# Performance work log

Measured on AMD Instinct MI355X. Metric: run time of the kernel, lower is better.

## Reference

```python
import jax, jax.numpy as jnp
import numpy as np

N = 4096
HID = 256
H = 4
D = HID // H  # 64
EDGE_DIM = 16
DEG = 32
E = N * DEG
EPS = 1e-5


def _layer_norm(x, g, b):
    m = jnp.mean(x, axis=-1, keepdims=True)
    v = jnp.mean((x - m) ** 2, axis=-1, keepdims=True)
    return (x - m) * jax.lax.rsqrt(v + EPS) * g + b


def setup_inputs() -> dict:
    key = jax.random.key(0)
    ks = jax.random.split(key, 16)
    s = 1.0 / np.sqrt(HID)
    x = jax.random.normal(ks[0], (N, HID), dtype=jnp.float32)
    # ring graph: every node is a src with DEG distinct neighbors -> no empty
    # softmax rows, no duplicate (src, dst) pairs
    src = jnp.repeat(jnp.arange(N, dtype=jnp.int64), DEG)
    dst = (src + jnp.tile(jnp.arange(1, DEG + 1, dtype=jnp.int64), N)) % N
    edge_index = jnp.stack([src, dst], axis=0)
    edge_attr = jax.random.normal(ks[1], (E, EDGE_DIM), dtype=jnp.float32)
    inp = {
        "x": x,
        "edge_index": edge_index,
        "edge_attr": edge_attr,
        "Wq": jax.random.uniform(ks[2], (HID, HID), jnp.float32, -s, s),
        "bq": jnp.zeros((HID,), jnp.float32),
        "Wk": jax.random.uniform(ks[3], (HID, HID), jnp.float32, -s, s),
        "bk": jnp.zeros((HID,), jnp.float32),
        "Wv": jax.random.uniform(ks[4], (HID, HID), jnp.float32, -s, s),
        "bv": jnp.zeros((HID,), jnp.float32),
        "Wo": jax.random.uniform(ks[5], (HID, HID), jnp.float32, -s, s),
        "bo": jnp.zeros((HID,), jnp.float32),
        "We": jax.random.uniform(ks[6], (EDGE_DIM, H), jnp.float32, -1.0 / np.sqrt(EDGE_DIM), 1.0 / np.sqrt(EDGE_DIM)),
        "be": jnp.zeros((H,), jnp.float32),
        "g1": jnp.ones((HID,), jnp.float32),
        "b1": jnp.zeros((HID,), jnp.float32),
        "g2": jnp.ones((HID,), jnp.float32),
        "b2": jnp.zeros((HID,), jnp.float32),
        "Wf1": jax.random.uniform(ks[7], (HID, 4 * HID), jnp.float32, -s, s),
        "bf1": jnp.zeros((4 * HID,), jnp.float32),
        "Wf2": jax.random.uniform(ks[8], (4 * HID, HID), jnp.float32, -1.0 / np.sqrt(4 * HID), 1.0 / np.sqrt(4 * HID)),
        "bf2": jnp.zeros((HID,), jnp.float32),
    }
    return inp


def reference(x, edge_index, edge_attr, Wq, bq, Wk, bk, Wv, bv, Wo, bo,
              We, be, g1, b1, g2, b2, Wf1, bf1, Wf2, bf2):
    src, dst = edge_index[0], edge_index[1]
    q = (x @ Wq + bq).reshape(N, H, D)
    k = (x @ Wk + bk).reshape(N, H, D)
    v = (x @ Wv + bv).reshape(N, H, D)
    edge_bias = edge_attr @ We + be                       # [E, H]
    dot = jnp.sum(q[src] * k[dst], axis=-1) / np.sqrt(D)  # [E, H]
    total_bias = dot + edge_bias                          # [E, H]
    # dense (H, N, N) logits, -inf everywhere except the E edges (as in the
    # original module)
    logits = jnp.full((H, N, N), -jnp.inf, dtype=x.dtype)
    logits = logits.at[:, src, dst].set(total_bias.T)
    attn = jax.nn.softmax(logits, axis=-1)                # [H, N, N]
    out = jnp.einsum('hnm,mhd->nhd', attn, v).reshape(N, HID)
    out = out @ Wo + bo
    x = _layer_norm(x + out, g1, b1)
    ffn = jax.nn.relu(x @ Wf1 + bf1) @ Wf2 + bf2
    x = _layer_norm(x + ffn, g2, b2)
    return x
```

## Files before the change

### kernel.cpp

```cpp
#include <hip/hip_runtime.h>
#include <cstddef>

#define N_NODES 4096
#define HIDDEN  256
#define NHEAD   4
#define DHEAD   64
#define EDGE_DIM 16
#define DEG     32
#define NEDGE   (N_NODES * DEG)
#define LN_EPS  1e-5f
#define QKV_STRIDE 768
#define KV_WIN  47

typedef short  s16x8 __attribute__((ext_vector_type(8)));
typedef float  f32x4 __attribute__((ext_vector_type(4)));
typedef unsigned short u16x8 __attribute__((ext_vector_type(8)));
typedef unsigned short u16x4 __attribute__((ext_vector_type(4)));

__device__ __forceinline__ unsigned short f2b(float f) {
    union { float f; unsigned u; } c{f};
    unsigned u = c.u;
    return (unsigned short)((u + 0x7fffu + ((u >> 16) & 1u)) >> 16);
}
__device__ __forceinline__ float b2f(unsigned short s) {
    union { unsigned u; float f; } c;
    c.u = ((unsigned)s) << 16;
    return c.f;
}
__device__ __forceinline__ int xcd_swz(int bid, int total) {
    const int q = total >> 3;
    return (bid & 7) * q + (bid >> 3);
}

__device__ __forceinline__ void pack_tile(const float* __restrict__ src,
                                          unsigned short* __restrict__ dst,
                                          int K, int Nn, int tt, int rowoff,
                                          float (*tile)[65], int tid) {
    const int tk = K / 64;
    const int k0 = (tt % tk) * 64, n0 = (tt / tk) * 64;

    const int kk = tid >> 2, nq = (tid & 3) * 16;
#pragma unroll
    for (int i = 0; i < 16; i += 4) {
        float4 vv = *(const float4*)&src[(size_t)(k0 + kk) * Nn + n0 + nq + i];
        tile[kk][nq + i + 0] = vv.x;
        tile[kk][nq + i + 1] = vv.y;
        tile[kk][nq + i + 2] = vv.z;
        tile[kk][nq + i + 3] = vv.w;
    }
    __syncthreads();
    const int nn = tid >> 2, kq = (tid & 3) * 16;
    unsigned short tmp[16];
#pragma unroll
    for (int i = 0; i < 16; ++i) tmp[i] = f2b(tile[kq + i][nn]);
    unsigned short* drow = dst + (size_t)(rowoff + n0 + nn) * K + k0 + kq;
    *(u16x8*)(drow + 0) = *(u16x8*)&tmp[0];
    *(u16x8*)(drow + 8) = *(u16x8*)&tmp[8];
}

__global__ __launch_bounds__(256) void pack_kernel(
    const float* __restrict__ Wq, const float* __restrict__ Wk,
    const float* __restrict__ Wv, const float* __restrict__ Wo,
    const float* __restrict__ Wf1, const float* __restrict__ Wf2,
    const float* __restrict__ bq, const float* __restrict__ bk,
    const float* __restrict__ bv,
    unsigned short* __restrict__ Wqkv_t, unsigned short* __restrict__ Wo_t,
    unsigned short* __restrict__ Wf1_t, unsigned short* __restrict__ Wf2_t,
    float* __restrict__ bias768) {
    const int b = blockIdx.x;
    const int tid = threadIdx.x;
    __shared__ float tile[64][65];

    if (b < 48) {
        int m = b / 16, tt = b % 16;
        const float* src = (m == 0) ? Wq : ((m == 1) ? Wk : Wv);
        pack_tile(src, Wqkv_t, 256, 256, tt, m * 256, tile, tid);
    } else if (b < 64) {
        pack_tile(Wo, Wo_t, 256, 256, b - 48, 0, tile, tid);
    } else if (b < 128) {
        pack_tile(Wf1, Wf1_t, 256, 1024, b - 64, 0, tile, tid);
    } else if (b < 192) {
        pack_tile(Wf2, Wf2_t, 1024, 256, b - 128, 0, tile, tid);
    } else {
        bias768[tid]       = bq[tid];
        bias768[256 + tid] = bk[tid];
        bias768[512 + tid] = bv[tid];
    }
}

__global__ __launch_bounds__(256) void gemm_qkv(const float* __restrict__ X,
                                                const unsigned short* __restrict__ Bt,
                                                const float* __restrict__ bias,
                                                unsigned short* __restrict__ Cout) {
    __shared__ unsigned short sA[64 * 64];
    __shared__ unsigned short sB[96 * 64];
    const int tid = threadIdx.x;
    const int wave = tid >> 6, lane = tid & 63;
    const int b2 = xcd_swz(blockIdx.x, 512);
    const int row0 = (b2 >> 3) * 64, col0 = (b2 & 7) * 96;
    const int wr = wave >> 1, wc = wave & 1;

    f32x4 acc[2][3] = {};

    const int ar  = tid >> 2;
    const int akb = (tid & 3) * 16;
    const int acb = akb * 2;
    const int axr = (ar & 7) << 4;
    const int aso0 = (ar * 128) | ((acb +  0) ^ axr);
    const int aso1 = (ar * 128) | ((acb + 16) ^ axr);

    float4 f0, f1, f2v, f3;
    s16x8 breg[3];

#define QKV_LOAD(KT)                                                          \
    {                                                                         \
        const float* Ap = X + (size_t)(row0 + ar) * 256 + (KT) * 64 + akb;    \
        f0  = *(const float4*)(Ap + 0);                                       \
        f1  = *(const float4*)(Ap + 4);                                       \
        f2v = *(const float4*)(Ap + 8);                                       \
        f3  = *(const float4*)(Ap + 12);                                      \
        const char* Bb = (const char*)Bt + ((size_t)col0 * 256 + (KT) * 64) * 2; \
        _Pragma("unroll")                                                     \
        for (int p = 0; p < 3; ++p) {                                         \
            const int lo = tid * 16 + p * 4096;                               \
            const int r = lo >> 7, c = lo & 127;                              \
            breg[p] = *(const s16x8*)(Bb + (size_t)r * 512 + c);              \
        }                                                                     \
    }

    QKV_LOAD(0);
#pragma unroll
    for (int kt = 0; kt < 4; ++kt) {
        if (kt) __syncthreads();
        u16x8 pa0 = {f2b(f0.x), f2b(f0.y), f2b(f0.z), f2b(f0.w),
                     f2b(f1.x), f2b(f1.y), f2b(f1.z), f2b(f1.w)};
        u16x8 pa1 = {f2b(f2v.x), f2b(f2v.y), f2b(f2v.z), f2b(f2v.w),
                     f2b(f3.x), f2b(f3.y), f2b(f3.z), f2b(f3.w)};
        *(u16x8*)((char*)sA + aso0) = pa0;
        *(u16x8*)((char*)sA + aso1) = pa1;
#pragma unroll
        for (int p = 0; p < 3; ++p) {
            const int lo = tid * 16 + p * 4096;
            const int r = lo >> 7, c = lo & 127;
            const int so = (lo & ~127) | (c ^ ((r & 7) << 4));
            *(s16x8*)((char*)sB + so) = breg[p];
        }
        __syncthreads();
        if (kt < 3) QKV_LOAD(kt + 1);

        const char* sAc = (const char*)sA;
        const char* sBc = (const char*)sB;
#pragma unroll
        for (int kk = 0; kk < 64; kk += 32) {
            const int koffb = (kk + ((lane >> 4) << 3)) * 2;
            s16x8 a[2], bfr[3];
#pragma unroll
            for (int m = 0; m < 2; ++m) {
                const int r = wr * 32 + m * 16 + (lane & 15);
                int off = r * 128 + koffb;
                off ^= (r & 7) << 4;
                a[m] = *(const s16x8*)(sAc + off);
            }
#pragma unroll
            for (int n = 0; n < 3; ++n) {
                const int c = wc * 48 + n * 16 + (lane & 15);
                int off = c * 128 + koffb;
                off ^= (c & 7) << 4;
                bfr[n] = *(const s16x8*)(sBc + off);
            }
#pragma unroll
            for (int m = 0; m < 2; ++m)
#pragma unroll
                for (int n = 0; n < 3; ++n)
                    acc[m][n] = __builtin_amdgcn_mfma_f32_16x16x32_bf16(
                        a[m], bfr[n], acc[m][n], 0, 0, 0);
        }
    }
#undef QKV_LOAD

    const int crow = row0 + wr * 32 + ((lane >> 4) << 2);
    const int ccol = col0 + wc * 48 + (lane & 15);
#pragma unroll
    for (int n = 0; n < 3; ++n) {
        const int c = ccol + n * 16;
        const float bv = bias[c];
#pragma unroll
        for (int m = 0; m < 2; ++m)
#pragma unroll
            for (int j = 0; j < 4; ++j)
                Cout[(size_t)(crow + m * 16 + j) * QKV_STRIDE + c] =
                    f2b(acc[m][n][j] + bv);
    }
}

__global__ __launch_bounds__(256) void gemm_ffn1(const unsigned short* __restrict__ A,
                                                 const unsigned short* __restrict__ Bt,
                                                 const float* __restrict__ bias,
                                                 unsigned short* __restrict__ Cout) {
    constexpr int K = 256;
    __shared__ unsigned short sA[64 * 64];
    __shared__ unsigned short sB[128 * 64];
    const int tid = threadIdx.x;
    const int wave = tid >> 6, lane = tid & 63;
    const int b2 = xcd_swz(blockIdx.x, 512);
    const int row0 = (b2 >> 3) * 64, col0 = (b2 & 7) * 128;
    const int wr = wave >> 1, wc = wave & 1;

    f32x4 acc[2][4] = {};

    const int lo0 = tid * 16, lo1 = lo0 + 4096;
    const int r0 = lo0 >> 7, c0 = lo0 & 127;
    const int r1 = lo1 >> 7, c1 = lo1 & 127;
    const int so0 = (lo0 & ~127) | (c0 ^ ((r0 & 7) << 4));
    const int so1 = (lo1 & ~127) | (c1 ^ ((r1 & 7) << 4));

    s16x8 a0r, a1r, breg[4];

#define F1_LOAD(KT)                                                           \
    {                                                                         \
        const char* Ab = (const char*)A + ((size_t)row0 * K + (KT) * 64) * 2; \
        a0r = *(const s16x8*)(Ab + (size_t)r0 * (K * 2) + c0);                \
        a1r = *(const s16x8*)(Ab + (size_t)r1 * (K * 2) + c1);                \
        const char* Bb = (const char*)Bt + ((size_t)col0 * K + (KT) * 64) * 2;\
        _Pragma("unroll")                                                     \
        for (int p = 0; p < 4; ++p) {                                         \
            const int lo = tid * 16 + p * 4096;                               \
            const int r = lo >> 7, c = lo & 127;                              \
            breg[p] = *(const s16x8*)(Bb + (size_t)r * (K * 2) + c);          \
        }                                                                     \
    }

    F1_LOAD(0);
#pragma unroll
    for (int kt = 0; kt < 4; ++kt) {
        if (kt) __syncthreads();
        *(s16x8*)((char*)sA + so0) = a0r;
        *(s16x8*)((char*)sA + so1) = a1r;
#pragma unroll
        for (int p = 0; p < 4; ++p) {
            const int lo = tid * 16 + p * 4096;
            const int r = lo >> 7, c = lo & 127;
            const int so = (lo & ~127) | (c ^ ((r & 7) << 4));
            *(s16x8*)((char*)sB + so) = breg[p];
        }
        __syncthreads();
        if (kt + 1 < 4) F1_LOAD(kt + 1);

        const char* sAc = (const char*)sA;
        const char* sBc = (const char*)sB;
#pragma unroll
        for (int kk = 0; kk < 64; kk += 32) {
            const int koffb = (kk + ((lane >> 4) << 3)) * 2;
            s16x8 a[2], bfr[4];
#pragma unroll
            for (int m = 0; m < 2; ++m) {
                const int r = wr * 32 + m * 16 + (lane & 15);
                int off = r * 128 + koffb;
                off ^= (r & 7) << 4;
                a[m] = *(const s16x8*)(sAc + off);
            }
#pragma unroll
            for (int n = 0; n < 4; ++n) {
                const int c = wc * 64 + n * 16 + (lane & 15);
                int off = c * 128 + koffb;
                off ^= (c & 7) << 4;
                bfr[n] = *(const s16x8*)(sBc + off);
            }
#pragma unroll
            for (int m = 0; m < 2; ++m)
#pragma unroll
                for (int n = 0; n < 4; ++n)
                    acc[m][n] = __builtin_amdgcn_mfma_f32_16x16x32_bf16(
                        a[m], bfr[n], acc[m][n], 0, 0, 0);
        }
    }
#undef F1_LOAD

    const int crow = row0 + wr * 32 + ((lane >> 4) << 2);
    const int ccol = col0 + wc * 64 + (lane & 15);
#pragma unroll
    for (int n = 0; n < 4; ++n) {
        const int c = ccol + n * 16;
        const float bv = bias[c];
#pragma unroll
        for (int m = 0; m < 2; ++m)
#pragma unroll
            for (int j = 0; j < 4; ++j) {
                const int r = crow + m * 16 + j;
                Cout[(size_t)r * 1024 + c] = f2b(fmaxf(acc[m][n][j] + bv, 0.f));
            }
    }
}

__global__ __launch_bounds__(256) void gemm_partial(const unsigned short* __restrict__ A,
                                                    const unsigned short* __restrict__ Bt,
                                                    float* __restrict__ part) {
    constexpr int KF = 1024;
    __shared__ unsigned short sA[64 * 64];
    __shared__ unsigned short sB[64 * 64];
    const int tid = threadIdx.x;
    const int wave = tid >> 6, lane = tid & 63;
    const int b2 = xcd_swz(blockIdx.x, 512);
    const int z = b2 >> 8;
    const int rem = b2 & 255;
    const int row0 = (rem >> 2) * 64, col0 = (rem & 3) * 64;
    const int wr = wave >> 1, wc = wave & 1;

    f32x4 acc[2][2] = {};

    const int lo0 = tid * 16;
    const int lo1 = lo0 + 4096;
    const int r0 = lo0 >> 7, c0 = lo0 & 127;
    const int r1 = lo1 >> 7, c1 = lo1 & 127;
    const int so0 = (lo0 & ~127) | (c0 ^ ((r0 & 7) << 4));
    const int so1 = (lo1 & ~127) | (c1 ^ ((r1 & 7) << 4));

    const char* Abase = (const char*)A + ((size_t)row0 * KF + z * 512) * 2;
    const char* Bbase = (const char*)Bt + ((size_t)col0 * KF + z * 512) * 2;

    s16x8 a0r, a1r, b0r, b1r;

#define GP_LOAD(KT)                                                           \
    {                                                                         \
        a0r = *(const s16x8*)(Abase + (KT) * 128 + (size_t)r0 * (KF * 2) + c0); \
        a1r = *(const s16x8*)(Abase + (KT) * 128 + (size_t)r1 * (KF * 2) + c1); \
        b0r = *(const s16x8*)(Bbase + (KT) * 128 + (size_t)r0 * (KF * 2) + c0); \
        b1r = *(const s16x8*)(Bbase + (KT) * 128 + (size_t)r1 * (KF * 2) + c1); \
    }

    GP_LOAD(0);
#pragma unroll
    for (int kt = 0; kt < 8; ++kt) {
        if (kt) __syncthreads();
        *(s16x8*)((char*)sA + so0) = a0r;
        *(s16x8*)((char*)sA + so1) = a1r;
        *(s16x8*)((char*)sB + so0) = b0r;
        *(s16x8*)((char*)sB + so1) = b1r;
        __syncthreads();
        if (kt + 1 < 8) GP_LOAD(kt + 1);

        const char* sAc = (const char*)sA;
        const char* sBc = (const char*)sB;
#pragma unroll
        for (int kk = 0; kk < 64; kk += 32) {
            const int koffb = (kk + ((lane >> 4) << 3)) * 2;
            s16x8 a[2], bfr[2];
#pragma unroll
            for (int m = 0; m < 2; ++m) {
                const int r = wr * 32 + m * 16 + (lane & 15);
                int off = r * 128 + koffb;
                off ^= (r & 7) << 4;
                a[m] = *(const s16x8*)(sAc + off);
            }
#pragma unroll
            for (int n = 0; n < 2; ++n) {
                const int c = wc * 32 + n * 16 + (lane & 15);
                int off = c * 128 + koffb;
                off ^= (c & 7) << 4;
                bfr[n] = *(const s16x8*)(sBc + off);
            }
#pragma unroll
            for (int m = 0; m < 2; ++m)
#pragma unroll
                for (int n = 0; n < 2; ++n)
                    acc[m][n] = __builtin_amdgcn_mfma_f32_16x16x32_bf16(
                        a[m], bfr[n], acc[m][n], 0, 0, 0);
        }
    }
#undef GP_LOAD

    const int crow = row0 + wr * 32 + ((lane >> 4) << 2);
    const int ccol = col0 + wc * 32 + (lane & 15);
    float* pz = part + (size_t)z * N_NODES * HIDDEN;
#pragma unroll
    for (int n = 0; n < 2; ++n) {
        const int c = ccol + n * 16;
#pragma unroll
        for (int m = 0; m < 2; ++m)
#pragma unroll
            for (int j = 0; j < 4; ++j)
                pz[(size_t)(crow + m * 16 + j) * HIDDEN + c] = acc[m][n][j];
    }
}

__global__ __launch_bounds__(256) void ln2_reduce(const float* __restrict__ part,
                                                  const unsigned short* __restrict__ yb,
                                                  const float* __restrict__ bf2,
                                                  const float* __restrict__ g2,
                                                  const float* __restrict__ b2,
                                                  float* __restrict__ out) {
    const int tid = threadIdx.x;
    const int row = blockIdx.x * 8 + (tid >> 5);
    const int cb = (tid & 31) * 8;
    const size_t rb = (size_t)row * HIDDEN;
    constexpr size_t ZS = (size_t)N_NODES * HIDDEN;

    u16x8 yv = *(const u16x8*)&yb[rb + cb];
    float vals[8];
#pragma unroll
    for (int q = 0; q < 2; ++q) {
        const int c = cb + q * 4;
        float4 vb = *(const float4*)&bf2[c];
        float4 s0 = *(const float4*)&part[0 * ZS + rb + c];
        float4 s1 = *(const float4*)&part[1 * ZS + rb + c];
        vals[q * 4 + 0] = b2f(yv[q * 4 + 0]) + vb.x + s0.x + s1.x;
        vals[q * 4 + 1] = b2f(yv[q * 4 + 1]) + vb.y + s0.y + s1.y;
        vals[q * 4 + 2] = b2f(yv[q * 4 + 2]) + vb.z + s0.z + s1.z;
        vals[q * 4 + 3] = b2f(yv[q * 4 + 3]) + vb.w + s0.w + s1.w;
    }
    float sm = 0.f, sq = 0.f;
#pragma unroll
    for (int i = 0; i < 8; ++i) { sm += vals[i]; sq = fmaf(vals[i], vals[i], sq); }
#pragma unroll
    for (int off = 16; off >= 1; off >>= 1) {
        sm += __shfl_xor(sm, off);
        sq += __shfl_xor(sq, off);
    }
    const float mean = sm * (1.f / HIDDEN);
    const float var  = sq * (1.f / HIDDEN) - mean * mean;
    const float inv  = rsqrtf(var + LN_EPS);
#pragma unroll
    for (int q = 0; q < 2; ++q) {
        const int c = cb + q * 4;
        float4 vg = *(const float4*)&g2[c];
        float4 vbb = *(const float4*)&b2[c];
        float4 o;
        o.x = (vals[q * 4 + 0] - mean) * inv * vg.x + vbb.x;
        o.y = (vals[q * 4 + 1] - mean) * inv * vg.y + vbb.y;
        o.z = (vals[q * 4 + 2] - mean) * inv * vg.z + vbb.z;
        o.w = (vals[q * 4 + 3] - mean) * inv * vg.w + vbb.w;
        *(float4*)&out[rb + c] = o;
    }
}

__global__ __launch_bounds__(512) void attn_oproj_ln(
    const unsigned short* __restrict__ qkv,
    const int* __restrict__ edge_dst,
    const float* __restrict__ edge_attr,
    const float* __restrict__ We, const float* __restrict__ be,
    const unsigned short* __restrict__ Wo_t,
    const float* __restrict__ bo,
    const float* __restrict__ x,
    const float* __restrict__ g, const float* __restrict__ b,
    unsigned short* __restrict__ yb) {
    __shared__ float sQ[16][260];
    __shared__ float sP[16][NHEAD][DEG];
    __shared__ int   sDst[16][DEG];
    __shared__ float sWe[EDGE_DIM * NHEAD];
    __shared__ unsigned short sKV[2][KV_WIN * 256];
    __shared__ unsigned short sA[16 * 256];
    __shared__ unsigned short sB[2][256 * 64];
    __shared__ float rs[16][8], rq[16][8];

    const int tid = threadIdx.x;
    const int wave = tid >> 6, lane = tid & 63;
    const int n0 = blockIdx.x * 16;

    {
        const int r = tid >> 5, e = (tid & 31) * 8;
        u16x8 v = *(const u16x8*)(qkv + (size_t)(n0 + r) * QKV_STRIDE + e);
#pragma unroll
        for (int i = 0; i < 8; ++i) sQ[r][e + i] = b2f(v[i]);
    }
    for (int t = tid; t < 2 * KV_WIN * 32; t += 512) {
        const int half = (t >= KV_WIN * 32) ? 1 : 0;
        const int tt = t - half * (KV_WIN * 32);
        const int rr = tt >> 5, c16 = tt & 31;
        const int gsrc = (n0 + 1 + rr) & (N_NODES - 1);
        u16x8 v = *(const u16x8*)(qkv + (size_t)gsrc * QKV_STRIDE +
                                  (half ? 512 : 256) + c16 * 8);
        const int so = rr * 512 + ((c16 ^ (rr & 7)) * 16);
        *(u16x8*)((char*)sKV[half] + so) = v;
    }
    if (tid < EDGE_DIM * NHEAD) sWe[tid] = We[tid];
    __syncthreads();

    {
        const int node = tid >> 5, j = tid & 31;
        const int dstj = edge_dst[(n0 + node) * DEG + j];
        sDst[node][j] = dstj;
        const int idx = (dstj - n0 - 1) & (N_NODES - 1);
        const char* krow = (const char*)sKV[0] + idx * 512;
        const int swz = (idx & 7);
        float lg[4];
#pragma unroll
        for (int h = 0; h < 4; ++h) {
            float dot = 0.f;
            const float* qh = &sQ[node][h * 64];
#pragma unroll
            for (int q8 = 0; q8 < 8; ++q8) {
                const int c16 = h * 8 + q8;
                u16x8 kv = *(const u16x8*)(krow + ((c16 ^ swz) * 16));
#pragma unroll
                for (int d = 0; d < 8; ++d)
                    dot = fmaf(qh[q8 * 8 + d], b2f(kv[d]), dot);
            }
            lg[h] = dot * 0.125f + be[h];
        }
        const float* ea_ = edge_attr + (size_t)((n0 + node) * DEG + j) * EDGE_DIM;
#pragma unroll
        for (int c = 0; c < EDGE_DIM; ++c) {
            const float eav = ea_[c];
#pragma unroll
            for (int h = 0; h < 4; ++h)
                lg[h] = fmaf(eav, sWe[c * NHEAD + h], lg[h]);
        }
#pragma unroll
        for (int h = 0; h < 4; ++h) {
            float mx = lg[h];
#pragma unroll
            for (int off = 16; off >= 1; off >>= 1)
                mx = fmaxf(mx, __shfl_xor(mx, off));
            float p = __expf(lg[h] - mx);
            float sum = p;
#pragma unroll
            for (int off = 16; off >= 1; off >>= 1)
                sum += __shfl_xor(sum, off);
            sP[node][h][j] = p / sum;
        }
    }
    __syncthreads();

    {
        const int node = tid >> 5, oct = tid & 31;
        const int h = oct >> 3;
        const int chunk = oct;
        float acc8[8] = {};
#pragma unroll 8
        for (int j = 0; j < DEG; ++j) {
            const float p = sP[node][h][j];
            const int idx = (sDst[node][j] - n0 - 1) & (N_NODES - 1);
            u16x8 vv = *(const u16x8*)((const char*)sKV[1] + idx * 512 +
                                       ((chunk ^ (idx & 7)) * 16));
#pragma unroll
            for (int i = 0; i < 8; ++i) acc8[i] = fmaf(p, b2f(vv[i]), acc8[i]);
        }
        u16x8 pk;
#pragma unroll
        for (int i = 0; i < 8; ++i) pk[i] = f2b(acc8[i]);
        const int so = node * 512 + ((oct * 16) ^ ((node & 7) << 4));
        *(u16x8*)((char*)sA + so) = pk;
    }

    s16x8 breg[4];
#define WO_LOAD(KT)                                                           \
    {                                                                         \
        _Pragma("unroll")                                                     \
        for (int p = 0; p < 4; ++p) {                                         \
            const int lo = tid * 16 + p * 8192;                               \
            const int r = lo >> 7, c = lo & 127;                              \
            breg[p] = *(const s16x8*)((const char*)Wo_t + (size_t)r * 512 +   \
                                      (KT) * 128 + c);                        \
        }                                                                     \
    }
#define WO_STORE(BUF)                                                         \
    {                                                                         \
        _Pragma("unroll")                                                     \
        for (int p = 0; p < 4; ++p) {                                         \
            const int lo = tid * 16 + p * 8192;                               \
            const int r = lo >> 7, c = lo & 127;                              \
            const int so = (lo & ~127) | (c ^ ((r & 7) << 4));                \
            *(s16x8*)((char*)sB[BUF] + so) = breg[p];                         \
        }                                                                     \
    }

    WO_LOAD(0);
    WO_STORE(0);
    __syncthreads();

    f32x4 acc[2] = {};
#pragma unroll
    for (int kt = 0; kt < 4; ++kt) {
        if (kt + 1 < 4) WO_LOAD(kt + 1);

        const char* sBc = (const char*)sB[kt & 1];
#pragma unroll
        for (int kk = 0; kk < 64; kk += 32) {
            const int lk = ((lane >> 4) << 3);
            s16x8 a;
            {
                const int r = lane & 15;
                const int koffb = (kt * 64 + kk + lk) * 2;
                a = *(const s16x8*)((const char*)sA + r * 512 +
                                    (koffb ^ ((r & 7) << 4)));
            }
            s16x8 bfr[2];
            const int boffb = (kk + lk) * 2;
#pragma unroll
            for (int n = 0; n < 2; ++n) {
                const int c = wave * 32 + n * 16 + (lane & 15);
                bfr[n] = *(const s16x8*)(sBc + c * 128 + (boffb ^ ((c & 7) << 4)));
            }
#pragma unroll
            for (int n = 0; n < 2; ++n)
                acc[n] = __builtin_amdgcn_mfma_f32_16x16x32_bf16(a, bfr[n], acc[n], 0, 0, 0);
        }

        if (kt + 1 < 4) {
            WO_STORE((kt + 1) & 1);
            __syncthreads();
        }
    }
#undef WO_LOAD
#undef WO_STORE

    const int rbase = ((lane >> 4) << 2);
    const int cbase = wave * 32 + (lane & 15);

    float sm[4] = {}, sq_[4] = {};
#pragma unroll
    for (int n = 0; n < 2; ++n) {
        const int c = cbase + n * 16;
        const float bv = bo[c];
#pragma unroll
        for (int j = 0; j < 4; ++j) {
            const int r = rbase + j;
            float v = acc[n][j] + bv + x[(size_t)(n0 + r) * HIDDEN + c];
            acc[n][j] = v;
            sm[j] += v;
            sq_[j] = fmaf(v, v, sq_[j]);
        }
    }
#pragma unroll
    for (int off = 8; off >= 1; off >>= 1) {
#pragma unroll
        for (int j = 0; j < 4; ++j) {
            sm[j] += __shfl_xor(sm[j], off);
            sq_[j] += __shfl_xor(sq_[j], off);
        }
    }
    if ((lane & 15) == 0) {
#pragma unroll
        for (int j = 0; j < 4; ++j) {
            rs[rbase + j][wave] = sm[j];
            rq[rbase + j][wave] = sq_[j];
        }
    }
    __syncthreads();

#pragma unroll
    for (int j = 0; j < 4; ++j) {
        const int r = rbase + j;
        float tot = 0.f, totq = 0.f;
#pragma unroll
        for (int w = 0; w < 8; ++w) { tot += rs[r][w]; totq += rq[r][w]; }
        const float mean = tot * (1.f / HIDDEN);
        const float var  = totq * (1.f / HIDDEN) - mean * mean;
        const float inv  = rsqrtf(var + LN_EPS);
#pragma unroll
        for (int n = 0; n < 2; ++n) {
            const int c = cbase + n * 16;
            const float res = (acc[n][j] - mean) * inv * g[c] + b[c];
            yb[(size_t)(n0 + r) * HIDDEN + c] = f2b(res);
        }
    }
}

extern "C" void kernel_launch(void* const* d_in, const int* in_sizes, int n_in,
                              void* d_out, int out_size, void* d_ws, size_t ws_size,
                              hipStream_t stream) {
    const float* x   = (const float*)d_in[0];
    const int*   ei  = (const int*)d_in[1];
    const float* ea  = (const float*)d_in[2];
    const float* Wq  = (const float*)d_in[3];
    const float* bq  = (const float*)d_in[4];
    const float* Wk  = (const float*)d_in[5];
    const float* bk  = (const float*)d_in[6];
    const float* Wv  = (const float*)d_in[7];
    const float* bv  = (const float*)d_in[8];
    const float* Wo  = (const float*)d_in[9];
    const float* bo  = (const float*)d_in[10];
    const float* We  = (const float*)d_in[11];
    const float* be  = (const float*)d_in[12];
    const float* g1  = (const float*)d_in[13];
    const float* b1  = (const float*)d_in[14];
    const float* g2  = (const float*)d_in[15];
    const float* b2  = (const float*)d_in[16];
    const float* Wf1 = (const float*)d_in[17];
    const float* bf1 = (const float*)d_in[18];
    const float* Wf2 = (const float*)d_in[19];
    const float* bf2 = (const float*)d_in[20];

    char* W = (char*)d_ws;
    unsigned short* Wqkv_t  = (unsigned short*)(W + (2u << 20));
    unsigned short* Wo_t    = (unsigned short*)(W + (2u << 20) + 384 * 1024);
    unsigned short* Wf1_t   = (unsigned short*)(W + (2u << 20) + 512 * 1024);
    unsigned short* Wf2_t   = (unsigned short*)(W + (2u << 20) + 1024 * 1024);
    float*          bias768 = (float*)(W + (2u << 20) + 1536 * 1024);
    unsigned short* qkvb    = (unsigned short*)(W + (4u << 20));
    unsigned short* h1b     = (unsigned short*)(W + (4u << 20));
    unsigned short* yb      = (unsigned short*)(W + (16u << 20));
    float*          part    = (float*)(W + (20u << 20));

    const dim3 blk(256);

    pack_kernel<<<193, blk, 0, stream>>>(Wq, Wk, Wv, Wo, Wf1, Wf2, bq, bk, bv,
                                         Wqkv_t, Wo_t, Wf1_t, Wf2_t, bias768);

    gemm_qkv<<<512, blk, 0, stream>>>(x, Wqkv_t, bias768, qkvb);

    attn_oproj_ln<<<N_NODES / 16, dim3(512), 0, stream>>>(
        qkvb, ei + NEDGE, ea, We, be, Wo_t, bo, x, g1, b1, yb);

    gemm_ffn1<<<512, blk, 0, stream>>>(yb, Wf1_t, bf1, h1b);

    gemm_partial<<<512, blk, 0, stream>>>(h1b, Wf2_t, part);

    ln2_reduce<<<N_NODES / 8, blk, 0, stream>>>(part, yb, bf2, g2, b2, (float*)d_out);
}
```

Measured before the change: 53.54 us.

## Read Wo fragments directly from global and alias sQ/sA to cut LDS

Removes the double-buffered shared-memory staging of Wo in the fused attention+O-proj+LN kernel, so MFMA B fragments are loaded straight from global (L2-resident) Wo_t. The sQ and sA buffers now share one shared-memory region. Launch bounds request 4 blocks per CU. This shrinks LDS use from roughly 130KB to about 64KB so more blocks can be resident, which should hide latency better. The trade-off is uncoalesced, strided global loads for B, and a possible race if sA is written while sQ is still being read without a barrier in between.

New measurement: 54.31 us. About the same (+1.4%).

```diff
diff --git a/kernel.cpp b/kernel.cpp
--- a/kernel.cpp
+++ b/kernel.cpp
@@ -433,7 +433,7 @@
     }
 }
 
-__global__ __launch_bounds__(512) void attn_oproj_ln(
+__global__ __launch_bounds__(512, 4) void attn_oproj_ln(
     const unsigned short* __restrict__ qkv,
     const int* __restrict__ edge_dst,
     const float* __restrict__ edge_attr,
@@ -443,14 +443,15 @@
     const float* __restrict__ x,
     const float* __restrict__ g, const float* __restrict__ b,
     unsigned short* __restrict__ yb) {
-    __shared__ float sQ[16][260];
+    __shared__ __align__(16) char uQA[16 * 260 * 4];
     __shared__ float sP[16][NHEAD][DEG];
     __shared__ int   sDst[16][DEG];
     __shared__ float sWe[EDGE_DIM * NHEAD];
     __shared__ unsigned short sKV[2][KV_WIN * 256];
-    __shared__ unsigned short sA[16 * 256];
-    __shared__ unsigned short sB[2][256 * 64];
     __shared__ float rs[16][8], rq[16][8];
+
+    float (*sQ)[260] = (float(*)[260])uQA;
+    unsigned short* sA = (unsigned short*)uQA;
 
     const int tid = threadIdx.x;
     const int wave = tid >> 6, lane = tid & 63;
@@ -541,68 +542,32 @@
         const int so = node * 512 + ((oct * 16) ^ ((node & 7) << 4));
         *(u16x8*)((char*)sA + so) = pk;
     }
-
-    s16x8 breg[4];
-#define WO_LOAD(KT)                                                           \
-    {                                                                         \
-        _Pragma("unroll")                                                     \
-        for (int p = 0; p < 4; ++p) {                                         \
-            const int lo = tid * 16 + p * 8192;                               \
-            const int r = lo >> 7, c = lo & 127;                              \
-            breg[p] = *(const s16x8*)((const char*)Wo_t + (size_t)r * 512 +   \
-                                      (KT) * 128 + c);                        \
-        }                                                                     \
-    }
-#define WO_STORE(BUF)                                                         \
-    {                                                                         \
-        _Pragma("unroll")                                                     \
-        for (int p = 0; p < 4; ++p) {                                         \
-            const int lo = tid * 16 + p * 8192;                               \
-            const int r = lo >> 7, c = lo & 127;                              \
-            const int so = (lo & ~127) | (c ^ ((r & 7) << 4));                \
-            *(s16x8*)((char*)sB[BUF] + so) = breg[p];                         \
-        }                                                                     \
-    }
-
-    WO_LOAD(0);
-    WO_STORE(0);
     __syncthreads();
 
     f32x4 acc[2] = {};
 #pragma unroll
     for (int kt = 0; kt < 4; ++kt) {
-        if (kt + 1 < 4) WO_LOAD(kt + 1);
-
-        const char* sBc = (const char*)sB[kt & 1];
 #pragma unroll
         for (int kk = 0; kk < 64; kk += 32) {
             const int lk = ((lane >> 4) << 3);
+            const int koffb = (kt * 64 + kk + lk) * 2;
             s16x8 a;
             {
                 const int r = lane & 15;
-                const int koffb = (kt * 64 + kk + lk) * 2;
                 a = *(const s16x8*)((const char*)sA + r * 512 +
                                     (koffb ^ ((r & 7) << 4)));
             }
             s16x8 bfr[2];
-            const int boffb = (kk + lk) * 2;
 #pragma unroll
             for (int n = 0; n < 2; ++n) {
                 const int c = wave * 32 + n * 16 + (lane & 15);
-                bfr[n] = *(const s16x8*)(sBc + c * 128 + (boffb ^ ((c & 7) << 4)));
+                bfr[n] = *(const s16x8*)((const char*)Wo_t + (size_t)c * 512 + koffb);
             }
 #pragma unroll
             for (int n = 0; n < 2; ++n)
                 acc[n] = __builtin_amdgcn_mfma_f32_16x16x32_bf16(a, bfr[n], acc[n], 0, 0, 0);
         }
-
-        if (kt + 1 < 4) {
-            WO_STORE((kt + 1) & 1);
-            __syncthreads();
-        }
-    }
-#undef WO_LOAD
-#undef WO_STORE
+    }
 
     const int rbase = ((lane >> 4) << 2);
     const int cbase = wave * 32 + (lane & 15);
```
